# Kernel tuning notes

Hardware: AMD Instinct MI355X
Metric: run time of the kernel (lower is better)

The kernel has to match this reference:

```python
import jax, jax.numpy as jnp
import numpy as np

B, T, D = 256, 512, 128   # batch, T_max, input_dim
Z, TR, EM, RH = 128, 256, 256, 512  # z_dim, trans_dim, emission_dim, rnn_dim


def _dkf_infer(x, y, eps_comb, eps_emit, rnn_Wih, rnn_Whh, rnn_bih, rnn_bhh, h0, zq0,
               tr_g1_W, tr_g1_b, tr_g2_W, tr_g2_b, tr_p1_W, tr_p1_b, tr_p2_W, tr_p2_b,
               tr_mu_W, tr_mu_b, tr_lv_W, tr_lv_b,
               cb_h_W, cb_h_b, cb_mu_W, cb_mu_b, cb_lv_W, cb_lv_b,
               em_h1_W, em_h1_b, em_h2_W, em_h2_b, em_mu_W, em_mu_b, em_logvar):
    b = x.shape[0]
    # --- nn.RNN (relu nonlinearity, batch_first), scanned time-major ---
    xw = jnp.einsum('btd,dh->tbh', x, rnn_Wih) + rnn_bih  # [T,B,RH] input projection hoisted out of scan

    def rnn_step(h, xw_t):
        h = jax.nn.relu(xw_t + h @ rnn_Whh + rnn_bhh)
        return h, h

    _, rnn_out = jax.lax.scan(rnn_step, jnp.broadcast_to(h0, (b, h0.shape[0])), xw)  # [T,B,RH]

    y_tm = jnp.swapaxes(y, 0, 1)  # [T,B,D]

    def step(z_prev, inp):
        h_rnn, yt, e_cb, e_em = inp
        # GatedTransition (infer only uses prior mu/logvar; its sample is discarded)
        gate = jax.nn.sigmoid(jax.nn.relu(z_prev @ tr_g1_W + tr_g1_b) @ tr_g2_W + tr_g2_b)
        prop = jax.nn.relu(z_prev @ tr_p1_W + tr_p1_b) @ tr_p2_W + tr_p2_b
        pr_mu = (1.0 - gate) * (z_prev @ tr_mu_W + tr_mu_b) + gate * prop
        pr_lv = jax.nn.relu(prop) @ tr_lv_W + tr_lv_b
        # Combiner + reparameterization
        hc = 0.5 * (jnp.tanh(z_prev @ cb_h_W + cb_h_b) + h_rnn)
        mu = hc @ cb_mu_W + cb_mu_b
        lv = hc @ cb_lv_W + cb_lv_b
        z_t = mu + e_cb * jnp.exp(0.5 * lv)
        # Emitter + reparameterization
        h1 = jax.nn.relu(z_t @ em_h1_W + em_h1_b)
        h2 = jax.nn.relu(h1 @ em_h2_W + em_h2_b)
        x_mu = h2 @ em_mu_W + em_mu_b
        x_t = x_mu + e_em * jnp.exp(0.5 * em_logvar)
        # KL(q || prior) summed over z, per batch element
        kl = jnp.sum(0.5 * (pr_lv - lv + (jnp.exp(lv) + (mu - pr_mu) ** 2) / jnp.exp(pr_lv) - 1.0), axis=1)
        # per-element MSE reduced over x_dim
        rec = jnp.mean((x_t - yt) ** 2, axis=1)
        return z_t, (kl, rec)

    z0 = jnp.broadcast_to(zq0, (b, zq0.shape[0]))
    _, (kl_states, rec_losses) = jax.lax.scan(step, z0, (rnn_out, y_tm, eps_comb, eps_emit))
    return jnp.stack([jnp.mean(rec_losses), jnp.mean(kl_states)])  # [rec_loss, kl_loss]


def setup_inputs() -> dict:
    key = jax.random.key(0)
    ks = iter(jax.random.split(key, 32))
    nrm = lambda shape, s=0.05: jax.random.normal(next(ks), shape, dtype=jnp.float32) * s
    z = lambda *shape: jnp.zeros(shape, jnp.float32)
    return dict(
        x=nrm((B, T, D), 1.0), y=nrm((B, T, D), 1.0),
        eps_comb=nrm((T, B, Z), 1.0), eps_emit=nrm((T, B, D), 1.0),
        rnn_Wih=nrm((D, RH)), rnn_Whh=nrm((RH, RH)), rnn_bih=z(RH), rnn_bhh=z(RH),
        h0=z(RH), zq0=z(Z),
        tr_g1_W=nrm((Z, TR)), tr_g1_b=z(TR), tr_g2_W=nrm((TR, Z)), tr_g2_b=z(Z),
        tr_p1_W=nrm((Z, TR)), tr_p1_b=z(TR), tr_p2_W=nrm((TR, Z)), tr_p2_b=z(Z),
        tr_mu_W=jnp.eye(Z, dtype=jnp.float32), tr_mu_b=z(Z),  # identity init as in torch code
        tr_lv_W=nrm((Z, Z)), tr_lv_b=z(Z),
        cb_h_W=nrm((Z, RH)), cb_h_b=z(RH),
        cb_mu_W=nrm((RH, Z)), cb_mu_b=z(Z),
        cb_lv_W=nrm((RH, Z)), cb_lv_b=z(Z),
        em_h1_W=nrm((Z, EM)), em_h1_b=z(EM),
        em_h2_W=nrm((EM, EM)), em_h2_b=z(EM),
        em_mu_W=nrm((EM, D)), em_mu_b=z(D),
        em_logvar=jnp.ones((D,), jnp.float32),  # nn.Parameter(torch.ones(input_dim))
    )


def reference(x, y, eps_comb, eps_emit, rnn_Wih, rnn_Whh, rnn_bih, rnn_bhh, h0, zq0,
              tr_g1_W, tr_g1_b, tr_g2_W, tr_g2_b, tr_p1_W, tr_p1_b, tr_p2_W, tr_p2_b,
              tr_mu_W, tr_mu_b, tr_lv_W, tr_lv_b,
              cb_h_W, cb_h_b, cb_mu_W, cb_mu_b, cb_lv_W, cb_lv_b,
              em_h1_W, em_h1_b, em_h2_W, em_h2_b, em_mu_W, em_mu_b, em_logvar):
    return _dkf_infer(x, y, eps_comb, eps_emit, rnn_Wih, rnn_Whh, rnn_bih, rnn_bhh, h0, zq0,
                      tr_g1_W, tr_g1_b, tr_g2_W, tr_g2_b, tr_p1_W, tr_p1_b, tr_p2_W, tr_p2_b,
                      tr_mu_W, tr_mu_b, tr_lv_W, tr_lv_b,
                      cb_h_W, cb_h_b, cb_mu_W, cb_mu_b, cb_lv_W, cb_lv_b,
                      em_h1_W, em_h1_b, em_h2_W, em_h2_b, em_mu_W, em_mu_b, em_logvar)
```

## Files before the change

### kernel.cpp

```cpp
#include <hip/hip_runtime.h>


#define T_LEN 512
#define BATCH 256
#define DIMX  128
#define ZDIM  128
#define RHD   512

typedef _Float16 f16;
typedef _Float16 f16x4 __attribute__((ext_vector_type(4)));
typedef _Float16 f16x8 __attribute__((ext_vector_type(8)));
typedef float    f32x4 __attribute__((ext_vector_type(4)));

#define MFMA16(a,b,c) __builtin_amdgcn_mfma_f32_16x16x32_f16((a),(b),(c),0,0,0)

#define PK_WIH  0u
#define PK_WHH  65536u
#define PK_G1   327680u
#define PK_G2   360448u
#define PK_P1   393216u
#define PK_P2   425984u
#define PK_TMU  458752u
#define PK_TLV  475136u
#define PK_CBH  491520u
#define PK_CBML 557056u
#define PK_E1   688128u
#define PK_E2   720896u
#define PK_EMU  786432u

#define WS_XW   0ull
#define WS_Z    (WS_XW  + 134217728ull)
#define WS_MU   (WS_Z   + 33619968ull)
#define WS_LV   (WS_MU  + 33554432ull)
#define WS_PK   (WS_LV  + 33554432ull)
#define WS_PART (WS_PK  + 1638400ull)
#define WS_END  (WS_PART + 16384ull)

__device__ __forceinline__ void ldsfence() {
  asm volatile("s_waitcnt lgkmcnt(0)" ::: "memory");
  __builtin_amdgcn_sched_barrier(0);
}

__device__ __forceinline__ void pin8(f16x8& v) {
  f32x4 t = __builtin_bit_cast(f32x4, v);
  asm volatile("" : "+v"(t));
  v = __builtin_bit_cast(f16x8, t);
}

template<int N>
__device__ __forceinline__ void zacc(f32x4* a) {
  f32x4 z = {0.f, 0.f, 0.f, 0.f};
#pragma unroll
  for (int i = 0; i < N; ++i) a[i] = z;
}

__device__ __forceinline__ f16x8 cvt8(const float* p) {
  float4 a = *(const float4*)p, b = *(const float4*)(p + 4);
  f16x8 r;
  r[0] = (f16)a.x; r[1] = (f16)a.y; r[2] = (f16)a.z; r[3] = (f16)a.w;
  r[4] = (f16)b.x; r[5] = (f16)b.y; r[6] = (f16)b.z; r[7] = (f16)b.w;
  return r;
}

template<int KS>
__device__ __forceinline__ void load_af(const f16* src, int sstr, int lane, f16x8* af) {
#pragma unroll
  for (int ks = 0; ks < KS; ++ks)
    af[ks] = *(const f16x8*)(src + (lane & 15) * sstr + ks * 32 + ((lane >> 4) << 3));
}

template<int KS, int NT>
__device__ __forceinline__ void gemm_regA(const f16x8* af, const f16* __restrict__ bp,
                                          int lane, f32x4* acc) {
#pragma unroll
  for (int ks = 0; ks < KS; ++ks)
#pragma unroll
    for (int j = 0; j < NT; ++j) {
      f16x8 bf = *(const f16x8*)(bp + (((size_t)(ks * NT + j)) << 9) + (lane << 3));
      acc[j] = MFMA16(af[ks], bf, acc[j]);
    }
}

template<int NT>
__device__ __forceinline__ void store_relu(const f32x4* acc, const float* __restrict__ bias,
                                           f16* dst, int dstr, int lane) {
  int colv = lane & 15, rb = (lane >> 4) << 2;
#pragma unroll
  for (int j = 0; j < NT; ++j)
#pragma unroll
    for (int r = 0; r < 4; ++r)
      dst[(rb + r) * dstr + j * 16 + colv] = (f16)fmaxf(acc[j][r] + bias[j * 16 + colv], 0.f);
}

__global__ void pack_kernel(const float* __restrict__ s1, const float* __restrict__ s2,
                            int nsplit, int K, int N, f16* __restrict__ dst) {
  int idx = blockIdx.x * 256 + threadIdx.x;
  if (idx >= K * N) return;
  int j = idx & 7, l = (idx >> 3) & 63, fi = idx >> 9;
  int NTt = N >> 4;
  int nt = fi % NTt, ks = fi / NTt;
  int k = ks * 32 + ((l >> 4) << 3) + j;
  int n = (nt << 4) + (l & 15);
  float v;
  if (n < nsplit) v = s1[(size_t)k * nsplit + n];
  else            v = s2[(size_t)k * (N - nsplit) + (n - nsplit)];
  dst[idx] = (f16)v;
}

__global__ __launch_bounds__(256) void xw_kernel(
    const float* __restrict__ x, const f16* __restrict__ pk,
    const float* __restrict__ bih, const float* __restrict__ bhh,
    f16* __restrict__ xw) {
  __shared__ float bs[512];
  const int tid = threadIdx.x, lane = tid & 63, w = tid >> 6;
  const int colv = lane & 15, l4 = lane >> 4;
  const int m0 = blockIdx.x * 64 + w * 16;
  const int t = m0 >> 8, b0 = m0 & 255;
  for (int i = tid; i < 512; i += 256) bs[i] = bih[i] + bhh[i];
  __syncthreads();
  f16x8 xB[4];
  const float* xr = x + ((size_t)(b0 + colv) * T_LEN + t) * DIMX;
#pragma unroll
  for (int ks = 0; ks < 4; ++ks) xB[ks] = cvt8(xr + ks * 32 + l4 * 8);
  f32x4 acc[32]; zacc<32>(acc);
#pragma unroll
  for (int ks = 0; ks < 4; ++ks)
#pragma unroll
    for (int mt = 0; mt < 32; ++mt)
      acc[mt] = MFMA16(*(const f16x8*)(pk + PK_WIH + ((size_t)(ks * 32 + mt) << 9) + (lane << 3)),
                       xB[ks], acc[mt]);
  f16* xo = xw + ((size_t)t * BATCH + b0 + colv) * RHD;
#pragma unroll
  for (int mt = 0; mt < 32; ++mt) {
    f16x4 v;
#pragma unroll
    for (int r = 0; r < 4; ++r) v[r] = (f16)(acc[mt][r] + bs[mt * 16 + l4 * 4 + r]);
    *(f16x4*)(xo + mt * 16 + l4 * 4) = v;
  }
}

__global__ __launch_bounds__(512, 2) void rnn_kernel(
    const f16* __restrict__ pk, const float* __restrict__ h0,
    f16* __restrict__ xw) {
  __shared__ __align__(16) f16 whh_lds[65536];
  __shared__ __align__(16) f16 h_st[16][520];
  const int tid = threadIdx.x, lane = tid & 63, w = tid >> 6;
  const int colv = lane & 15, l4 = lane >> 4;
  const int b0 = blockIdx.x * 16;

  {
    const uint4* src = (const uint4*)(pk + PK_WHH + 196608u);
    for (int i = tid; i < 8192; i += 512) ((uint4*)whh_lds)[i] = src[i];
  }
  f16x8 whhA[4][12];
#pragma unroll
  for (int mt = 0; mt < 4; ++mt)
#pragma unroll
    for (int ks = 0; ks < 12; ++ks) {
      whhA[mt][ks] = *(const f16x8*)(pk + PK_WHH +
          ((size_t)(ks * 32 + 4 * w + mt) << 9) + (lane << 3));
      pin8(whhA[mt][ks]);
    }

  for (int i = tid; i < 16 * RHD; i += 512) h_st[i >> 9][i & 511] = (f16)h0[i & 511];
  __syncthreads();

  const int off0 = (4 * w) * 16 + l4 * 4;
  f16* xp = xw + (size_t)(b0 + colv) * RHD;
  f16x4 xwc[4], xwn[4];
#pragma unroll
  for (int mt = 0; mt < 4; ++mt) xwc[mt] = *(const f16x4*)(xp + off0 + mt * 16);

#pragma unroll 1
  for (int t = 0; t < T_LEN; ++t) {
    f16* xpn = (t < T_LEN - 1) ? (xp + (size_t)BATCH * RHD) : xp;
#pragma unroll
    for (int mt = 0; mt < 4; ++mt) xwn[mt] = *(const f16x4*)(xpn + off0 + mt * 16);

    f32x4 acc[4]; zacc<4>(acc);
#pragma unroll
    for (int kc = 0; kc < 6; ++kc) {
      f16x8 B2[2];
#pragma unroll
      for (int kk = 0; kk < 2; ++kk)
        B2[kk] = *(const f16x8*)&h_st[colv][(kc * 2 + kk) * 32 + l4 * 8];
#pragma unroll
      for (int kk = 0; kk < 2; ++kk)
#pragma unroll
        for (int mt = 0; mt < 4; ++mt)
          acc[mt] = MFMA16(whhA[mt][kc * 2 + kk], B2[kk], acc[mt]);
    }
#pragma unroll
    for (int kc = 0; kc < 2; ++kc) {
      f16x8 B2[2];
#pragma unroll
      for (int kk = 0; kk < 2; ++kk)
        B2[kk] = *(const f16x8*)&h_st[colv][(12 + kc * 2 + kk) * 32 + l4 * 8];
#pragma unroll
      for (int kk = 0; kk < 2; ++kk)
#pragma unroll
        for (int mt = 0; mt < 4; ++mt)
          acc[mt] = MFMA16(*(const f16x8*)(whh_lds +
              ((((kc * 2 + kk) * 32 + 4 * w + mt) << 6) + lane) * 8), B2[kk], acc[mt]);
    }
    __syncthreads();
#pragma unroll
    for (int mt = 0; mt < 4; ++mt) {
      f16x4 h4;
#pragma unroll
      for (int r = 0; r < 4; ++r)
        h4[r] = (f16)fmaxf(acc[mt][r] + (float)xwc[mt][r], 0.f);
      *(f16x4*)&h_st[colv][(4 * w + mt) * 16 + l4 * 4] = h4;
      *(f16x4*)(xp + off0 + mt * 16) = h4;
    }
    __syncthreads();
    xp = xpn;
#pragma unroll
    for (int mt = 0; mt < 4; ++mt) xwc[mt] = xwn[mt];
  }
}

__global__ __launch_bounds__(512, 2) void zscan_kernel(
    const f16* __restrict__ pk, const f16* __restrict__ rnn_out,
    const float* __restrict__ chb, const float* __restrict__ cmb,
    const float* __restrict__ clb, const float* __restrict__ zq0,
    const float* __restrict__ eps_comb,
    f16* __restrict__ z_all, f16* __restrict__ mu_all, f16* __restrict__ lv_all) {
  __shared__ __align__(16) f16 cbh_lds[65536];
  __shared__ __align__(16) f16 hc_st[16][520];
  __shared__ __align__(16) f16 z_st[16][136];
  __shared__ __align__(16) f16 m_st[16][264];
  const int tid = threadIdx.x, lane = tid & 63, w = tid >> 6;
  const int colv = lane & 15, l4 = lane >> 4;
  const int b0 = blockIdx.x * 16;

  {
    const uint4* src = (const uint4*)(pk + PK_CBH);
    for (int i = tid; i < 8192; i += 512) ((uint4*)cbh_lds)[i] = src[i];
  }
  f16x8 cbmlA[2][16];
#pragma unroll
  for (int mt = 0; mt < 2; ++mt)
#pragma unroll
    for (int ks = 0; ks < 16; ++ks) {
      cbmlA[mt][ks] = *(const f16x8*)(pk + PK_CBML +
          ((size_t)(ks * 16 + 2 * w + mt) << 9) + (lane << 3));
      pin8(cbmlA[mt][ks]);
    }

  float chbv[4][4];
#pragma unroll
  for (int mt = 0; mt < 4; ++mt)
#pragma unroll
    for (int r = 0; r < 4; ++r)
      chbv[mt][r] = chb[(4 * w + mt) * 16 + l4 * 4 + r];
  const int be = tid >> 5, d0 = (tid & 31) * 4;
  const float4 cmbv = *(const float4*)(cmb + d0);
  const float4 clbv = *(const float4*)(clb + d0);

  for (int i = tid; i < 16 * ZDIM; i += 512) {
    f16 zv = (f16)zq0[i & 127];
    z_st[i >> 7][i & 127] = zv;
    z_all[(size_t)(b0 + (i >> 7)) * ZDIM + (i & 127)] = zv;
  }
  __syncthreads();

  const int hoff = (4 * w) * 16 + l4 * 4;
  const f16* hp = rnn_out + (size_t)(b0 + colv) * RHD;
  const float* epp = eps_comb + (size_t)(b0 + be) * ZDIM + d0;
  f16x4 hvc[4], hvn[4];
  float4 epc, epn;
#pragma unroll
  for (int mt = 0; mt < 4; ++mt) hvc[mt] = *(const f16x4*)(hp + hoff + mt * 16);
  epc = *(const float4*)epp;

#pragma unroll 1
  for (int t = 0; t < T_LEN; ++t) {
    const f16* hpn = (t < T_LEN - 1) ? (hp + (size_t)BATCH * RHD) : hp;
    const float* eppn = (t < T_LEN - 1) ? (epp + (size_t)BATCH * ZDIM) : epp;
#pragma unroll
    for (int mt = 0; mt < 4; ++mt) hvn[mt] = *(const f16x4*)(hpn + hoff + mt * 16);
    epn = *(const float4*)eppn;

    f16x8 zB[4];
#pragma unroll
    for (int ks = 0; ks < 4; ++ks)
      zB[ks] = *(const f16x8*)&z_st[colv][ks * 32 + l4 * 8];
    f32x4 a1[4]; zacc<4>(a1);
#pragma unroll
    for (int ks = 0; ks < 4; ++ks)
#pragma unroll
      for (int mt = 0; mt < 4; ++mt)
        a1[mt] = MFMA16(*(const f16x8*)(cbh_lds +
            (((ks * 32 + 4 * w + mt) << 6) + lane) * 8), zB[ks], a1[mt]);
#pragma unroll
    for (int mt = 0; mt < 4; ++mt) {
      f16x4 hc4;
#pragma unroll
      for (int r = 0; r < 4; ++r) {
        float cs = a1[mt][r] + chbv[mt][r];
        float tt = __builtin_amdgcn_exp2f(cs * 2.885390082f);
        float th = 1.f - 2.f * __builtin_amdgcn_rcpf(tt + 1.f);
        hc4[r] = (f16)(0.5f * (th + (float)hvc[mt][r]));
      }
      *(f16x4*)&hc_st[colv][(4 * w + mt) * 16 + l4 * 4] = hc4;
    }
    __syncthreads();

    f32x4 a2[2]; zacc<2>(a2);
#pragma unroll
    for (int kc = 0; kc < 8; ++kc) {
      f16x8 hcB[2];
#pragma unroll
      for (int kk = 0; kk < 2; ++kk)
        hcB[kk] = *(const f16x8*)&hc_st[colv][(kc * 2 + kk) * 32 + l4 * 8];
#pragma unroll
      for (int kk = 0; kk < 2; ++kk)
#pragma unroll
        for (int mt = 0; mt < 2; ++mt)
          a2[mt] = MFMA16(cbmlA[mt][kc * 2 + kk], hcB[kk], a2[mt]);
    }
#pragma unroll
    for (int mt = 0; mt < 2; ++mt) {
      f16x4 v;
#pragma unroll
      for (int r = 0; r < 4; ++r) v[r] = (f16)a2[mt][r];
      *(f16x4*)&m_st[colv][(2 * w + mt) * 16 + l4 * 4] = v;
    }
    __syncthreads();

    {
      f16x4 muf = *(const f16x4*)&m_st[be][d0];
      f16x4 lvf = *(const f16x4*)&m_st[be][128 + d0];
      float epv[4] = {epc.x, epc.y, epc.z, epc.w};
      float cmv[4] = {cmbv.x, cmbv.y, cmbv.z, cmbv.w};
      float clv[4] = {clbv.x, clbv.y, clbv.z, clbv.w};
      f16x4 z4, mu4, lv4;
#pragma unroll
      for (int r = 0; r < 4; ++r) {
        float mu = (float)muf[r] + cmv[r];
        float lv = (float)lvf[r] + clv[r];
        float zv = mu + epv[r] * __builtin_amdgcn_exp2f(lv * 0.7213475204f);
        z4[r] = (f16)zv; mu4[r] = (f16)mu; lv4[r] = (f16)lv;
      }
      *(f16x4*)&z_st[be][d0] = z4;
      size_t o = ((size_t)t * BATCH + b0 + be) * ZDIM + d0;
      *(f16x4*)(z_all + o + (size_t)BATCH * ZDIM) = z4;
      *(f16x4*)(mu_all + o) = mu4;
      *(f16x4*)(lv_all + o) = lv4;
    }
    __syncthreads();
    hp = hpn; epp = eppn;
#pragma unroll
    for (int mt = 0; mt < 4; ++mt) hvc[mt] = hvn[mt];
    epc = epn;
  }
}

__global__ __launch_bounds__(256) void dpar_kernel(
    const f16* __restrict__ z_all, const f16* __restrict__ mu_all,
    const f16* __restrict__ lv_all, const float* __restrict__ y,
    const float* __restrict__ eps_emit, const f16* __restrict__ pk,
    const float* __restrict__ g1b, const float* __restrict__ g2b,
    const float* __restrict__ p1b, const float* __restrict__ p2b,
    const float* __restrict__ tmub, const float* __restrict__ tlvb,
    const float* __restrict__ e1b, const float* __restrict__ e2b,
    const float* __restrict__ emub, const float* __restrict__ em_logvar,
    float* __restrict__ partials) {
  __shared__ __align__(16) f16 sb256[4][16 * 264];
  __shared__ __align__(16) f16 sb128[4][16 * 136];
  __shared__ float wsum[4][2];
  const int tid = threadIdx.x, lane = tid & 63, w = tid >> 6;
  const int colv = lane & 15, rb = (lane >> 4) << 2;
  const int m0 = blockIdx.x * 64 + w * 16;
  const int t = m0 >> 8, b0 = m0 & 255;
  f16* B256 = &sb256[w][0];
  f16* B128 = &sb128[w][0];

  f16x8 zp[4], zt[4];
  const f16* zpr = z_all + ((size_t)t * BATCH + b0) * ZDIM;
#pragma unroll
  for (int ks = 0; ks < 4; ++ks) {
    zp[ks] = *(const f16x8*)(zpr + (size_t)colv * ZDIM + ks * 32 + ((lane >> 4) << 3));
    zt[ks] = *(const f16x8*)(zpr + (size_t)BATCH * ZDIM + (size_t)colv * ZDIM + ks * 32 + ((lane >> 4) << 3));
  }

  f32x4 a16[16], a8[8];
  f16x8 af[8], af4[4];
  zacc<16>(a16); gemm_regA<4, 16>(zp, pk + PK_G1, lane, a16);
  store_relu<16>(a16, g1b, B256, 264, lane); ldsfence();
  load_af<8>(B256, 264, lane, af); ldsfence();
  zacc<8>(a8); gemm_regA<8, 8>(af, pk + PK_G2, lane, a8);
  f32x4 gate[8];
#pragma unroll
  for (int j = 0; j < 8; ++j)
#pragma unroll
    for (int r = 0; r < 4; ++r)
      gate[j][r] = 1.f / (1.f + expf(-(a8[j][r] + g2b[j * 16 + colv])));
  zacc<16>(a16); gemm_regA<4, 16>(zp, pk + PK_P1, lane, a16);
  store_relu<16>(a16, p1b, B256, 264, lane); ldsfence();
  load_af<8>(B256, 264, lane, af); ldsfence();
  zacc<8>(a8); gemm_regA<8, 8>(af, pk + PK_P2, lane, a8);
  f32x4 prop[8];
#pragma unroll
  for (int j = 0; j < 8; ++j)
#pragma unroll
    for (int r = 0; r < 4; ++r) {
      float v = a8[j][r] + p2b[j * 16 + colv];
      prop[j][r] = v;
      B128[(rb + r) * 136 + j * 16 + colv] = (f16)fmaxf(v, 0.f);
    }
  ldsfence();
  zacc<8>(a8); gemm_regA<4, 8>(zp, pk + PK_TMU, lane, a8);
  f32x4 prmu[8];
#pragma unroll
  for (int j = 0; j < 8; ++j)
#pragma unroll
    for (int r = 0; r < 4; ++r) {
      float gg = gate[j][r];
      prmu[j][r] = (1.f - gg) * (a8[j][r] + tmub[j * 16 + colv]) + gg * prop[j][r];
    }
  load_af<4>(B128, 136, lane, af4); ldsfence();
  zacc<8>(a8); gemm_regA<4, 8>(af4, pk + PK_TLV, lane, a8);
  f32x4 prlv[8];
#pragma unroll
  for (int j = 0; j < 8; ++j)
#pragma unroll
    for (int r = 0; r < 4; ++r) prlv[j][r] = a8[j][r] + tlvb[j * 16 + colv];
  zacc<16>(a16); gemm_regA<4, 16>(zt, pk + PK_E1, lane, a16);
  store_relu<16>(a16, e1b, B256, 264, lane); ldsfence();
  load_af<8>(B256, 264, lane, af); ldsfence();
  zacc<16>(a16); gemm_regA<8, 16>(af, pk + PK_E2, lane, a16);
  store_relu<16>(a16, e2b, B256, 264, lane); ldsfence();
  load_af<8>(B256, 264, lane, af); ldsfence();
  zacc<8>(a8); gemm_regA<8, 8>(af, pk + PK_EMU, lane, a8);
  float srec = 0.f, skl = 0.f;
#pragma unroll
  for (int j = 0; j < 8; ++j)
#pragma unroll
    for (int r = 0; r < 4; ++r) {
      int row = rb + r, n = j * 16 + colv;
      size_t tb = (size_t)t * BATCH + b0 + row;
      float xt = a8[j][r] + emub[n] + eps_emit[tb * DIMX + n] * expf(0.5f * em_logvar[n]);
      float dy = xt - y[((size_t)(b0 + row) * T_LEN + t) * DIMX + n];
      srec += dy * dy;
      float m_ = (float)mu_all[tb * ZDIM + n], l_ = (float)lv_all[tb * ZDIM + n];
      float dm = m_ - prmu[j][r];
      skl += 0.5f * (prlv[j][r] - l_ + (expf(l_) + dm * dm) * expf(-prlv[j][r]) - 1.f);
    }
#pragma unroll
  for (int off = 32; off; off >>= 1) {
    srec += __shfl_xor(srec, off);
    skl += __shfl_xor(skl, off);
  }
  if (lane == 0) { wsum[w][0] = srec; wsum[w][1] = skl; }
  __syncthreads();
  if (tid == 0) {
    partials[blockIdx.x * 2 + 0] = wsum[0][0] + wsum[1][0] + wsum[2][0] + wsum[3][0];
    partials[blockIdx.x * 2 + 1] = wsum[0][1] + wsum[1][1] + wsum[2][1] + wsum[3][1];
  }
}

__global__ void finalize_kernel(const float* __restrict__ partials, float* __restrict__ out) {
  __shared__ float sm[256][2];
  int tid = threadIdx.x;
  float r = 0.f, kk = 0.f;
  for (int i = tid; i < 2048; i += 256) {
    r += partials[2 * i];
    kk += partials[2 * i + 1];
  }
  sm[tid][0] = r; sm[tid][1] = kk;
  __syncthreads();
  for (int off = 128; off; off >>= 1) {
    if (tid < off) { sm[tid][0] += sm[tid + off][0]; sm[tid][1] += sm[tid + off][1]; }
    __syncthreads();
  }
  if (tid == 0) {
    out[0] = sm[0][0] / (131072.f * 128.f);
    out[1] = sm[0][1] / 131072.f;
  }
}

extern "C" void kernel_launch(void* const* d_in, const int* in_sizes, int n_in,
                              void* d_out, int out_size, void* d_ws, size_t ws_size,
                              hipStream_t stream) {
  (void)in_sizes; (void)n_in; (void)out_size;
  const float* x        = (const float*)d_in[0];
  const float* y        = (const float*)d_in[1];
  const float* eps_comb = (const float*)d_in[2];
  const float* eps_emit = (const float*)d_in[3];
  const float* wih = (const float*)d_in[4];
  const float* whh = (const float*)d_in[5];
  const float* bih = (const float*)d_in[6];
  const float* bhh = (const float*)d_in[7];
  const float* h0  = (const float*)d_in[8];
  const float* zq0 = (const float*)d_in[9];
  const float* g1W = (const float*)d_in[10]; const float* g1b = (const float*)d_in[11];
  const float* g2W = (const float*)d_in[12]; const float* g2b = (const float*)d_in[13];
  const float* p1W = (const float*)d_in[14]; const float* p1b = (const float*)d_in[15];
  const float* p2W = (const float*)d_in[16]; const float* p2b = (const float*)d_in[17];
  const float* tmuW = (const float*)d_in[18]; const float* tmub = (const float*)d_in[19];
  const float* tlvW = (const float*)d_in[20]; const float* tlvb = (const float*)d_in[21];
  const float* chW = (const float*)d_in[22]; const float* chb = (const float*)d_in[23];
  const float* cmW = (const float*)d_in[24]; const float* cmb = (const float*)d_in[25];
  const float* clW = (const float*)d_in[26]; const float* clb = (const float*)d_in[27];
  const float* e1W = (const float*)d_in[28]; const float* e1b = (const float*)d_in[29];
  const float* e2W = (const float*)d_in[30]; const float* e2b = (const float*)d_in[31];
  const float* emW = (const float*)d_in[32]; const float* emb = (const float*)d_in[33];
  const float* elv = (const float*)d_in[34];

  char* ws = (char*)d_ws;
  f16*  xw      = (f16*)(ws + WS_XW);
  f16*  z_all   = (f16*)(ws + WS_Z);
  f16*  mu_all  = (f16*)(ws + WS_MU);
  f16*  lv_all  = (f16*)(ws + WS_LV);
  f16*  pk      = (f16*)(ws + WS_PK);
  float* partials = (float*)(ws + WS_PART);
  float* out = (float*)d_out;
  if (ws_size < WS_END) return;

#define PACK(S1, S2, NS_, K, N, OFF) \
  pack_kernel<<<dim3(((K) * (N)) / 256), dim3(256), 0, stream>>>(S1, S2, NS_, K, N, pk + (OFF))
  PACK(wih, wih, 512, 128, 512, PK_WIH);
  PACK(whh, whh, 512, 512, 512, PK_WHH);
  PACK(g1W, g1W, 256, 128, 256, PK_G1);
  PACK(g2W, g2W, 128, 256, 128, PK_G2);
  PACK(p1W, p1W, 256, 128, 256, PK_P1);
  PACK(p2W, p2W, 128, 256, 128, PK_P2);
  PACK(tmuW, tmuW, 128, 128, 128, PK_TMU);
  PACK(tlvW, tlvW, 128, 128, 128, PK_TLV);
  PACK(chW, chW, 512, 128, 512, PK_CBH);
  PACK(cmW, clW, 128, 512, 256, PK_CBML);
  PACK(e1W, e1W, 256, 128, 256, PK_E1);
  PACK(e2W, e2W, 256, 256, 256, PK_E2);
  PACK(emW, emW, 128, 256, 128, PK_EMU);
#undef PACK

  xw_kernel<<<dim3(2048), dim3(256), 0, stream>>>(x, pk, bih, bhh, xw);
  rnn_kernel<<<dim3(16), dim3(512), 0, stream>>>(pk, h0, xw);
  zscan_kernel<<<dim3(16), dim3(512), 0, stream>>>(pk, xw, chb, cmb, clb, zq0,
                                                   eps_comb, z_all, mu_all, lv_all);
  dpar_kernel<<<dim3(2048), dim3(256), 0, stream>>>(z_all, mu_all, lv_all, y, eps_emit, pk,
                                                    g1b, g2b, p1b, p2b, tmub, tlvb, e1b, e2b,
                                                    emb, elv, partials);
  finalize_kernel<<<dim3(1), dim3(256), 0, stream>>>(partials, out);
}
```

Baseline: 3.109 ms.

## Swizzle LDS state, lighter barriers, register-resident combiner weights, single pack launch

Replaces the padded LDS state buffers in the RNN and z-scan loops with XOR-swizzled layouts, and swaps __syncthreads for a lighter lgkmcnt-wait plus s_barrier. The z-scan now keeps the combiner-hidden weights in registers and moves part of the mu/lv weights into LDS, folding their bias into the matmul epilogue. The thirteen pack launches are merged into one table-driven kernel. Extra __syncthreads are added in dpar around shared scratch reuse, which adds barrier cost there but guards against races.

```diff
diff --git a/kernel.cpp b/kernel.cpp
--- a/kernel.cpp
+++ b/kernel.cpp
@@ -41,6 +41,12 @@
   __builtin_amdgcn_sched_barrier(0);
 }
 
+__device__ __forceinline__ void lbar() {
+  asm volatile("s_waitcnt lgkmcnt(0)" ::: "memory");
+  __builtin_amdgcn_s_barrier();
+  asm volatile("" ::: "memory");
+}
+
 __device__ __forceinline__ void pin8(f16x8& v) {
   f32x4 t = __builtin_bit_cast(f32x4, v);
   asm volatile("" : "+v"(t));
@@ -62,6 +68,13 @@
   return r;
 }
 
+__device__ __forceinline__ int swz(int row, int col) {
+  return (row << 9) + (col ^ ((row & 7) << 3));
+}
+__device__ __forceinline__ int swz128(int row, int col) {
+  return (row << 7) + (col ^ ((row & 7) << 3));
+}
+
 template<int KS>
 __device__ __forceinline__ void load_af(const f16* src, int sstr, int lane, f16x8* af) {
 #pragma unroll
@@ -92,19 +105,26 @@
       dst[(rb + r) * dstr + j * 16 + colv] = (f16)fmaxf(acc[j][r] + bias[j * 16 + colv], 0.f);
 }
 
-__global__ void pack_kernel(const float* __restrict__ s1, const float* __restrict__ s2,
-                            int nsplit, int K, int N, f16* __restrict__ dst) {
-  int idx = blockIdx.x * 256 + threadIdx.x;
-  if (idx >= K * N) return;
+struct PackEnt { const float* s1; const float* s2; int nsplit, K, N; unsigned dst, wg0; };
+struct PackTab { PackEnt e[13]; };
+
+__global__ void pack_all_kernel(PackTab tb, f16* __restrict__ pk) {
+  int i = 0;
+#pragma unroll
+  for (int k = 1; k < 13; ++k)
+    if (blockIdx.x >= tb.e[k].wg0) i = k;
+  const PackEnt& E = tb.e[i];
+  int idx = (blockIdx.x - E.wg0) * 256 + threadIdx.x;
+  if (idx >= E.K * E.N) return;
   int j = idx & 7, l = (idx >> 3) & 63, fi = idx >> 9;
-  int NTt = N >> 4;
+  int NTt = E.N >> 4;
   int nt = fi % NTt, ks = fi / NTt;
   int k = ks * 32 + ((l >> 4) << 3) + j;
   int n = (nt << 4) + (l & 15);
   float v;
-  if (n < nsplit) v = s1[(size_t)k * nsplit + n];
-  else            v = s2[(size_t)k * (N - nsplit) + (n - nsplit)];
-  dst[idx] = (f16)v;
+  if (n < E.nsplit) v = E.s1[(size_t)k * E.nsplit + n];
+  else              v = E.s2[(size_t)k * (E.N - E.nsplit) + (n - E.nsplit)];
+  pk[E.dst + idx] = (f16)v;
 }
 
 __global__ __launch_bounds__(256) void xw_kernel(
@@ -143,7 +163,7 @@
     const f16* __restrict__ pk, const float* __restrict__ h0,
     f16* __restrict__ xw) {
   __shared__ __align__(16) f16 whh_lds[65536];
-  __shared__ __align__(16) f16 h_st[16][520];
+  __shared__ __align__(16) f16 h_st[16 * 512];
   const int tid = threadIdx.x, lane = tid & 63, w = tid >> 6;
   const int colv = lane & 15, l4 = lane >> 4;
   const int b0 = blockIdx.x * 16;
@@ -162,7 +182,8 @@
       pin8(whhA[mt][ks]);
     }
 
-  for (int i = tid; i < 16 * RHD; i += 512) h_st[i >> 9][i & 511] = (f16)h0[i & 511];
+  for (int i = tid; i < 16 * RHD; i += 512)
+    h_st[swz(i >> 9, i & 511)] = (f16)h0[i & 511];
   __syncthreads();
 
   const int off0 = (4 * w) * 16 + l4 * 4;
@@ -183,7 +204,7 @@
       f16x8 B2[2];
 #pragma unroll
       for (int kk = 0; kk < 2; ++kk)
-        B2[kk] = *(const f16x8*)&h_st[colv][(kc * 2 + kk) * 32 + l4 * 8];
+        B2[kk] = *(const f16x8*)&h_st[swz(colv, (kc * 2 + kk) * 32 + l4 * 8)];
 #pragma unroll
       for (int kk = 0; kk < 2; ++kk)
 #pragma unroll
@@ -195,7 +216,7 @@
       f16x8 B2[2];
 #pragma unroll
       for (int kk = 0; kk < 2; ++kk)
-        B2[kk] = *(const f16x8*)&h_st[colv][(12 + kc * 2 + kk) * 32 + l4 * 8];
+        B2[kk] = *(const f16x8*)&h_st[swz(colv, (12 + kc * 2 + kk) * 32 + l4 * 8)];
 #pragma unroll
       for (int kk = 0; kk < 2; ++kk)
 #pragma unroll
@@ -203,17 +224,17 @@
           acc[mt] = MFMA16(*(const f16x8*)(whh_lds +
               ((((kc * 2 + kk) * 32 + 4 * w + mt) << 6) + lane) * 8), B2[kk], acc[mt]);
     }
-    __syncthreads();
+    lbar();
 #pragma unroll
     for (int mt = 0; mt < 4; ++mt) {
       f16x4 h4;
 #pragma unroll
       for (int r = 0; r < 4; ++r)
         h4[r] = (f16)fmaxf(acc[mt][r] + (float)xwc[mt][r], 0.f);
-      *(f16x4*)&h_st[colv][(4 * w + mt) * 16 + l4 * 4] = h4;
+      *(f16x4*)&h_st[swz(colv, off0 + mt * 16)] = h4;
       *(f16x4*)(xp + off0 + mt * 16) = h4;
     }
-    __syncthreads();
+    lbar();
     xp = xpn;
 #pragma unroll
     for (int mt = 0; mt < 4; ++mt) xwc[mt] = xwn[mt];
@@ -226,41 +247,56 @@
     const float* __restrict__ clb, const float* __restrict__ zq0,
     const float* __restrict__ eps_comb,
     f16* __restrict__ z_all, f16* __restrict__ mu_all, f16* __restrict__ lv_all) {
-  __shared__ __align__(16) f16 cbh_lds[65536];
-  __shared__ __align__(16) f16 hc_st[16][520];
-  __shared__ __align__(16) f16 z_st[16][136];
+  __shared__ __align__(16) f16 cbml_lds[32768];
+  __shared__ __align__(16) f16 hc_st[16 * 512];
+  __shared__ __align__(16) f16 z_st[16 * 128];
   __shared__ __align__(16) f16 m_st[16][264];
   const int tid = threadIdx.x, lane = tid & 63, w = tid >> 6;
   const int colv = lane & 15, l4 = lane >> 4;
   const int b0 = blockIdx.x * 16;
 
   {
-    const uint4* src = (const uint4*)(pk + PK_CBH);
-    for (int i = tid; i < 8192; i += 512) ((uint4*)cbh_lds)[i] = src[i];
-  }
-  f16x8 cbmlA[2][16];
+    const uint4* src = (const uint4*)(pk + PK_CBML + 98304u);
+    for (int i = tid; i < 4096; i += 512) ((uint4*)cbml_lds)[i] = src[i];
+  }
+  f16x8 cbhA[4][4];
+#pragma unroll
+  for (int mt = 0; mt < 4; ++mt)
+#pragma unroll
+    for (int ks = 0; ks < 4; ++ks) {
+      cbhA[mt][ks] = *(const f16x8*)(pk + PK_CBH +
+          ((size_t)(ks * 32 + 4 * w + mt) << 9) + (lane << 3));
+      pin8(cbhA[mt][ks]);
+    }
+  f16x8 cbmlA[2][12];
 #pragma unroll
   for (int mt = 0; mt < 2; ++mt)
 #pragma unroll
-    for (int ks = 0; ks < 16; ++ks) {
+    for (int ks = 0; ks < 12; ++ks) {
       cbmlA[mt][ks] = *(const f16x8*)(pk + PK_CBML +
           ((size_t)(ks * 16 + 2 * w + mt) << 9) + (lane << 3));
       pin8(cbmlA[mt][ks]);
     }
 
-  float chbv[4][4];
+  f16x4 chbv[4];
 #pragma unroll
   for (int mt = 0; mt < 4; ++mt)
 #pragma unroll
     for (int r = 0; r < 4; ++r)
-      chbv[mt][r] = chb[(4 * w + mt) * 16 + l4 * 4 + r];
+      chbv[mt][r] = (f16)chb[(4 * w + mt) * 16 + l4 * 4 + r];
+  float mbias[2][4];
+#pragma unroll
+  for (int mt = 0; mt < 2; ++mt)
+#pragma unroll
+    for (int r = 0; r < 4; ++r) {
+      int d = (2 * w + mt) * 16 + l4 * 4 + r;
+      mbias[mt][r] = (d < 128) ? cmb[d] : clb[d - 128];
+    }
   const int be = tid >> 5, d0 = (tid & 31) * 4;
-  const float4 cmbv = *(const float4*)(cmb + d0);
-  const float4 clbv = *(const float4*)(clb + d0);
 
   for (int i = tid; i < 16 * ZDIM; i += 512) {
     f16 zv = (f16)zq0[i & 127];
-    z_st[i >> 7][i & 127] = zv;
+    z_st[swz128(i >> 7, i & 127)] = zv;
     z_all[(size_t)(b0 + (i >> 7)) * ZDIM + (i & 127)] = zv;
   }
   __syncthreads();
@@ -269,51 +305,48 @@
   const f16* hp = rnn_out + (size_t)(b0 + colv) * RHD;
   const float* epp = eps_comb + (size_t)(b0 + be) * ZDIM + d0;
   f16x4 hvc[4], hvn[4];
-  float4 epc, epn;
 #pragma unroll
   for (int mt = 0; mt < 4; ++mt) hvc[mt] = *(const f16x4*)(hp + hoff + mt * 16);
-  epc = *(const float4*)epp;
 
 #pragma unroll 1
   for (int t = 0; t < T_LEN; ++t) {
     const f16* hpn = (t < T_LEN - 1) ? (hp + (size_t)BATCH * RHD) : hp;
-    const float* eppn = (t < T_LEN - 1) ? (epp + (size_t)BATCH * ZDIM) : epp;
 #pragma unroll
     for (int mt = 0; mt < 4; ++mt) hvn[mt] = *(const f16x4*)(hpn + hoff + mt * 16);
-    epn = *(const float4*)eppn;
+    float4 ep = *(const float4*)epp;
+    epp += (size_t)BATCH * ZDIM;
 
     f16x8 zB[4];
 #pragma unroll
     for (int ks = 0; ks < 4; ++ks)
-      zB[ks] = *(const f16x8*)&z_st[colv][ks * 32 + l4 * 8];
+      zB[ks] = *(const f16x8*)&z_st[swz128(colv, ks * 32 + l4 * 8)];
     f32x4 a1[4]; zacc<4>(a1);
 #pragma unroll
     for (int ks = 0; ks < 4; ++ks)
 #pragma unroll
       for (int mt = 0; mt < 4; ++mt)
-        a1[mt] = MFMA16(*(const f16x8*)(cbh_lds +
-            (((ks * 32 + 4 * w + mt) << 6) + lane) * 8), zB[ks], a1[mt]);
+        a1[mt] = MFMA16(cbhA[mt][ks], zB[ks], a1[mt]);
 #pragma unroll
     for (int mt = 0; mt < 4; ++mt) {
       f16x4 hc4;
 #pragma unroll
       for (int r = 0; r < 4; ++r) {
-        float cs = a1[mt][r] + chbv[mt][r];
+        float cs = a1[mt][r] + (float)chbv[mt][r];
         float tt = __builtin_amdgcn_exp2f(cs * 2.885390082f);
         float th = 1.f - 2.f * __builtin_amdgcn_rcpf(tt + 1.f);
         hc4[r] = (f16)(0.5f * (th + (float)hvc[mt][r]));
       }
-      *(f16x4*)&hc_st[colv][(4 * w + mt) * 16 + l4 * 4] = hc4;
-    }
-    __syncthreads();
+      *(f16x4*)&hc_st[swz(colv, hoff + mt * 16)] = hc4;
+    }
+    lbar();
 
     f32x4 a2[2]; zacc<2>(a2);
 #pragma unroll
-    for (int kc = 0; kc < 8; ++kc) {
+    for (int kc = 0; kc < 6; ++kc) {
       f16x8 hcB[2];
 #pragma unroll
       for (int kk = 0; kk < 2; ++kk)
-        hcB[kk] = *(const f16x8*)&hc_st[colv][(kc * 2 + kk) * 32 + l4 * 8];
+        hcB[kk] = *(const f16x8*)&hc_st[swz(colv, (kc * 2 + kk) * 32 + l4 * 8)];
 #pragma unroll
       for (int kk = 0; kk < 2; ++kk)
 #pragma unroll
@@ -321,39 +354,47 @@
           a2[mt] = MFMA16(cbmlA[mt][kc * 2 + kk], hcB[kk], a2[mt]);
     }
 #pragma unroll
+    for (int kc = 0; kc < 2; ++kc) {
+      f16x8 hcB[2];
+#pragma unroll
+      for (int kk = 0; kk < 2; ++kk)
+        hcB[kk] = *(const f16x8*)&hc_st[swz(colv, (12 + kc * 2 + kk) * 32 + l4 * 8)];
+#pragma unroll
+      for (int kk = 0; kk < 2; ++kk)
+#pragma unroll
+        for (int mt = 0; mt < 2; ++mt)
+          a2[mt] = MFMA16(*(const f16x8*)(cbml_lds +
+              ((((kc * 2 + kk) * 16 + 2 * w + mt) << 6) + lane) * 8), hcB[kk], a2[mt]);
+    }
+#pragma unroll
     for (int mt = 0; mt < 2; ++mt) {
       f16x4 v;
 #pragma unroll
-      for (int r = 0; r < 4; ++r) v[r] = (f16)a2[mt][r];
+      for (int r = 0; r < 4; ++r) v[r] = (f16)(a2[mt][r] + mbias[mt][r]);
       *(f16x4*)&m_st[colv][(2 * w + mt) * 16 + l4 * 4] = v;
     }
-    __syncthreads();
+    lbar();
 
     {
       f16x4 muf = *(const f16x4*)&m_st[be][d0];
       f16x4 lvf = *(const f16x4*)&m_st[be][128 + d0];
-      float epv[4] = {epc.x, epc.y, epc.z, epc.w};
-      float cmv[4] = {cmbv.x, cmbv.y, cmbv.z, cmbv.w};
-      float clv[4] = {clbv.x, clbv.y, clbv.z, clbv.w};
-      f16x4 z4, mu4, lv4;
+      float epv[4] = {ep.x, ep.y, ep.z, ep.w};
+      f16x4 z4;
 #pragma unroll
       for (int r = 0; r < 4; ++r) {
-        float mu = (float)muf[r] + cmv[r];
-        float lv = (float)lvf[r] + clv[r];
-        float zv = mu + epv[r] * __builtin_amdgcn_exp2f(lv * 0.7213475204f);
-        z4[r] = (f16)zv; mu4[r] = (f16)mu; lv4[r] = (f16)lv;
+        float mu = (float)muf[r], lv = (float)lvf[r];
+        z4[r] = (f16)(mu + epv[r] * __builtin_amdgcn_exp2f(lv * 0.7213475204f));
       }
-      *(f16x4*)&z_st[be][d0] = z4;
+      *(f16x4*)&z_st[swz128(be, d0)] = z4;
       size_t o = ((size_t)t * BATCH + b0 + be) * ZDIM + d0;
       *(f16x4*)(z_all + o + (size_t)BATCH * ZDIM) = z4;
-      *(f16x4*)(mu_all + o) = mu4;
-      *(f16x4*)(lv_all + o) = lv4;
-    }
-    __syncthreads();
-    hp = hpn; epp = eppn;
+      *(f16x4*)(mu_all + o) = muf;
+      *(f16x4*)(lv_all + o) = lvf;
+    }
+    lbar();
+    hp = hpn;
 #pragma unroll
     for (int mt = 0; mt < 4; ++mt) hvc[mt] = hvn[mt];
-    epc = epn;
   }
 }
 
@@ -390,6 +431,7 @@
   zacc<16>(a16); gemm_regA<4, 16>(zp, pk + PK_G1, lane, a16);
   store_relu<16>(a16, g1b, B256, 264, lane); ldsfence();
   load_af<8>(B256, 264, lane, af); ldsfence();
+  __syncthreads();
   zacc<8>(a8); gemm_regA<8, 8>(af, pk + PK_G2, lane, a8);
   f32x4 gate[8];
 #pragma unroll
@@ -397,9 +439,11 @@
 #pragma unroll
     for (int r = 0; r < 4; ++r)
       gate[j][r] = 1.f / (1.f + expf(-(a8[j][r] + g2b[j * 16 + colv])));
+  __syncthreads();
   zacc<16>(a16); gemm_regA<4, 16>(zp, pk + PK_P1, lane, a16);
   store_relu<16>(a16, p1b, B256, 264, lane); ldsfence();
   load_af<8>(B256, 264, lane, af); ldsfence();
+  __syncthreads();
   zacc<8>(a8); gemm_regA<8, 8>(af, pk + PK_P2, lane, a8);
   f32x4 prop[8];
 #pragma unroll
@@ -411,6 +455,7 @@
       B128[(rb + r) * 136 + j * 16 + colv] = (f16)fmaxf(v, 0.f);
     }
   ldsfence();
+  __syncthreads();
   zacc<8>(a8); gemm_regA<4, 8>(zp, pk + PK_TMU, lane, a8);
   f32x4 prmu[8];
 #pragma unroll
@@ -421,18 +466,22 @@
       prmu[j][r] = (1.f - gg) * (a8[j][r] + tmub[j * 16 + colv]) + gg * prop[j][r];
     }
   load_af<4>(B128, 136, lane, af4); ldsfence();
+  __syncthreads();
   zacc<8>(a8); gemm_regA<4, 8>(af4, pk + PK_TLV, lane, a8);
   f32x4 prlv[8];
 #pragma unroll
   for (int j = 0; j < 8; ++j)
 #pragma unroll
     for (int r = 0; r < 4; ++r) prlv[j][r] = a8[j][r] + tlvb[j * 16 + colv];
+  __syncthreads();
   zacc<16>(a16); gemm_regA<4, 16>(zt, pk + PK_E1, lane, a16);
   store_relu<16>(a16, e1b, B256, 264, lane); ldsfence();
   load_af<8>(B256, 264, lane, af); ldsfence();
+  __syncthreads();
   zacc<16>(a16); gemm_regA<8, 16>(af, pk + PK_E2, lane, a16);
   store_relu<16>(a16, e2b, B256, 264, lane); ldsfence();
   load_af<8>(B256, 264, lane, af); ldsfence();
+  __syncthreads();
   zacc<8>(a8); gemm_regA<8, 8>(af, pk + PK_EMU, lane, a8);
   float srec = 0.f, skl = 0.f;
 #pragma unroll
@@ -519,8 +568,10 @@
   float* out = (float*)d_out;
   if (ws_size < WS_END) return;
 
-#define PACK(S1, S2, NS_, K, N, OFF) \
-  pack_kernel<<<dim3(((K) * (N)) / 256), dim3(256), 0, stream>>>(S1, S2, NS_, K, N, pk + (OFF))
+  PackTab tb;
+  unsigned wg = 0; int ei = 0;
+#define PACK(S1, S2, NS_, K_, N_, OFF) \
+  tb.e[ei] = PackEnt{S1, S2, NS_, K_, N_, OFF, wg}; wg += (unsigned)((K_) * (N_)) / 256; ++ei;
   PACK(wih, wih, 512, 128, 512, PK_WIH);
   PACK(whh, whh, 512, 512, 512, PK_WHH);
   PACK(g1W, g1W, 256, 128, 256, PK_G1);
@@ -535,6 +586,7 @@
   PACK(e2W, e2W, 256, 256, 256, PK_E2);
   PACK(emW, emW, 128, 256, 128, PK_EMU);
 #undef PACK
+  pack_all_kernel<<<dim3(wg), dim3(256), 0, stream>>>(tb, pk);
 
   xw_kernel<<<dim3(2048), dim3(256), 0, stream>>>(x, pk, bih, bhh, xw);
   rnn_kernel<<<dim3(16), dim3(512), 0, stream>>>(pk, h0, xw);
```

Result: slower. 3.422 ms (+10.1%).
